# Optimization experiments

Measured on AMD Instinct MI355X. Metric: run time of the kernel, lower is better.

## Reference

```python
import jax, jax.numpy as jnp
import numpy as np

H = 32          # encoding_size
VC = 128        # char vocab (both languages)
TC = 24         # max chars per word
NW = 4096       # words per sentence side


def lstm_cell(x_t, h, c, Wih, Whh, b):
    g = x_t @ Wih.T + h @ Whh.T + b
    i, f, gg, o = jnp.split(g, 4, axis=-1)
    c2 = jax.nn.sigmoid(f) * c + jax.nn.sigmoid(i) * jnp.tanh(gg)
    h2 = jax.nn.sigmoid(o) * jnp.tanh(c2)
    return h2, c2


def char_lstm_final(x, lens, Wih, Whh, b):
    """x: [N, T, V] packed char embeddings, lens: [N]. Returns final h [N, H].
    Mask-gated scan reproduces 'final hidden state at each word's true length'."""
    N, T, _ = x.shape
    Hh = Whh.shape[1]
    xt = jnp.swapaxes(x, 0, 1)                 # [T, N, V]
    ts = jnp.arange(T)

    def step(carry, inp):
        h, c = carry
        x_t, t = inp
        h2, c2 = lstm_cell(x_t, h, c, Wih, Whh, b)
        m = (t < lens)[:, None]
        return (jnp.where(m, h2, h), jnp.where(m, c2, c)), None

    z = jnp.zeros((N, Hh), x.dtype)
    (h, _), _ = jax.lax.scan(step, (z, z), (xt, ts))
    return h


def lstm_seq(xs, Wih, Whh, b):
    """xs: [T, D] (batch 1). Returns all hidden states [T, H]."""
    Hh = Whh.shape[1]

    def step(carry, x_t):
        h, c = carry
        h2, c2 = lstm_cell(x_t, h, c, Wih, Whh, b)
        return (h2, c2), h2

    z = jnp.zeros((Hh,), xs.dtype)
    _, ys = jax.lax.scan(step, (z, z), xs)
    return ys


def bilstm(xs, Wf_ih, Wf_hh, bf, Wb_ih, Wb_hh, bb):
    fwd = lstm_seq(xs, Wf_ih, Wf_hh, bf)
    bwd = lstm_seq(xs[::-1], Wb_ih, Wb_hh, bb)[::-1]
    return jnp.concatenate([fwd, bwd], axis=-1)   # [T, 2H]


def setup_inputs() -> dict:
    key = jax.random.key(0)
    ks = jax.random.split(key, 32)
    s = 0.1
    inp = {
        'e_chars': jax.random.randint(ks[0], (NW, TC), 0, VC, dtype=jnp.int32),
        'e_lens': jax.random.randint(ks[1], (NW,), 1, TC + 1, dtype=jnp.int32),
        'f_chars': jax.random.randint(ks[2], (NW, TC), 0, VC, dtype=jnp.int32),
        'f_lens': jax.random.randint(ks[3], (NW,), 1, TC + 1, dtype=jnp.int32),
        'diag': jax.random.uniform(ks[4], (NW, NW), dtype=jnp.float32),
        'embed_e': jax.random.normal(ks[5], (VC, VC), jnp.float32) * s,
        'embed_f': jax.random.normal(ks[6], (VC, VC), jnp.float32) * s,
        'e_char_Wih': jax.random.normal(ks[7], (4 * H, VC), jnp.float32) * s,
        'e_char_Whh': jax.random.normal(ks[8], (4 * H, H), jnp.float32) * s,
        'e_char_b': jax.random.normal(ks[9], (4 * H,), jnp.float32) * s,
        'f_char_Wih': jax.random.normal(ks[10], (4 * H, VC), jnp.float32) * s,
        'f_char_Whh': jax.random.normal(ks[11], (4 * H, H), jnp.float32) * s,
        'f_char_b': jax.random.normal(ks[12], (4 * H,), jnp.float32) * s,
        'e_fwd_Wih': jax.random.normal(ks[13], (4 * H, H), jnp.float32) * s,
        'e_fwd_Whh': jax.random.normal(ks[14], (4 * H, H), jnp.float32) * s,
        'e_fwd_b': jax.random.normal(ks[15], (4 * H,), jnp.float32) * s,
        'e_bwd_Wih': jax.random.normal(ks[16], (4 * H, H), jnp.float32) * s,
        'e_bwd_Whh': jax.random.normal(ks[17], (4 * H, H), jnp.float32) * s,
        'e_bwd_b': jax.random.normal(ks[18], (4 * H,), jnp.float32) * s,
        'f_fwd_Wih': jax.random.normal(ks[19], (4 * H, H), jnp.float32) * s,
        'f_fwd_Whh': jax.random.normal(ks[20], (4 * H, H), jnp.float32) * s,
        'f_fwd_b': jax.random.normal(ks[21], (4 * H,), jnp.float32) * s,
        'f_bwd_Wih': jax.random.normal(ks[22], (4 * H, H), jnp.float32) * s,
        'f_bwd_Whh': jax.random.normal(ks[23], (4 * H, H), jnp.float32) * s,
        'f_bwd_b': jax.random.normal(ks[24], (4 * H,), jnp.float32) * s,
    }
    return inp


def reference(e_chars, e_lens, f_chars, f_lens, diag,
              embed_e, embed_f,
              e_char_Wih, e_char_Whh, e_char_b,
              f_char_Wih, f_char_Whh, f_char_b,
              e_fwd_Wih, e_fwd_Whh, e_fwd_b,
              e_bwd_Wih, e_bwd_Whh, e_bwd_b,
              f_fwd_Wih, f_fwd_Whh, f_fwd_b,
              f_bwd_Wih, f_bwd_Whh, f_bwd_b):
    # per-word char-LSTM encodes (packed, mask-gated) -> [NW, H]
    e_seq = char_lstm_final(embed_e[e_chars], e_lens, e_char_Wih, e_char_Whh, e_char_b)
    f_seq = char_lstm_final(embed_f[f_chars], f_lens, f_char_Wih, f_char_Whh, f_char_b)
    # word-level bi-LSTM + sigmoid (module's self.tanh is nn.Sigmoid) -> [NW, 2H]
    e_enc = jax.nn.sigmoid(bilstm(e_seq, e_fwd_Wih, e_fwd_Whh, e_fwd_b,
                                  e_bwd_Wih, e_bwd_Whh, e_bwd_b))
    f_enc = jax.nn.sigmoid(bilstm(f_seq, f_fwd_Wih, f_fwd_Whh, f_fwd_b,
                                  f_bwd_Wih, f_bwd_Whh, f_bwd_b))
    # score_ij[i, j] = f_enc[i] . e_enc[j]  (single batched matmul; diag is unused, as in source)
    return f_enc @ e_enc.T
```

## Files before the change

### kernel.cpp

```cpp
#include <hip/hip_runtime.h>

#define kNW 4096
#define kTC 24
#define kCL 8
#define kBURN 32

typedef float v2f __attribute__((ext_vector_type(2)));
typedef int   v2i __attribute__((ext_vector_type(2)));

#define XE_OFF   0u
#define WH_OFF   32768u
#define ENC_OFF  2392064u

__device__ __forceinline__ float fsig(float x){
  return __builtin_amdgcn_rcpf(1.f + __builtin_amdgcn_exp2f(-1.44269504f * x));
}
__device__ __forceinline__ float ftanh_(float x){
  return fmaf(2.f, __builtin_amdgcn_rcpf(1.f + __builtin_amdgcn_exp2f(-2.88539008f * x)), -1.f);
}
__device__ __forceinline__ float rdlane(float v, int l){
  return __int_as_float(__builtin_amdgcn_readlane(__float_as_int(v), l));
}
__device__ __forceinline__ float xswap_lo2hi(float m){
#if defined(__has_builtin)
#if __has_builtin(__builtin_amdgcn_permlane32_swap)
  v2i r = __builtin_amdgcn_permlane32_swap(__float_as_int(m), __float_as_int(m), false, false);
  float a = __int_as_float(r.x), b = __int_as_float(r.y);
  return (a == m) ? b : a;
#else
  return __shfl(m, (int)(threadIdx.x & 31), 64);
#endif
#else
  return __shfl(m, (int)(threadIdx.x & 31), 64);
#endif
}

__global__ __launch_bounds__(256) void k_tables(
    const float* __restrict__ embed_e, const float* __restrict__ embed_f,
    const float* __restrict__ Wih_e, const float* __restrict__ b_e,
    const float* __restrict__ Wih_f, const float* __restrict__ b_f,
    float* __restrict__ ws)
{
  int lane = threadIdx.x & 63;
  int wv   = threadIdx.x >> 6;
  int gw   = blockIdx.x * 4 + wv;
  int side = gw >> 11;
  int c    = (gw & 2047) >> 4;
  int g0   = (gw & 15) * 8;
  const float* er = (side ? embed_f : embed_e) + c * 128;
  const float* Wih = side ? Wih_f : Wih_e;
  const float* bb  = side ? b_f   : b_e;
  float* X = ws + XE_OFF + side * 16384 + c * 128;

  float ea = er[lane], eb = er[lane + 64];
  #pragma unroll
  for (int i = 0; i < 8; ++i){
    const float* wr = Wih + (g0 + i) * 128;
    float p = ea * wr[lane] + eb * wr[lane + 64];
    #pragma unroll
    for (int m = 1; m < 64; m <<= 1) p += __shfl_xor(p, m, 64);
    if (lane == 0) X[g0 + i] = bb[g0 + i] + p;
  }
}

__global__ __launch_bounds__(64)
void k_char(
    const int* __restrict__ e_chars, const int* __restrict__ e_lens,
    const int* __restrict__ f_chars, const int* __restrict__ f_lens,
    const float* __restrict__ Whh_e, const float* __restrict__ Whh_f,
    float* __restrict__ ws)
{
  int side = blockIdx.y;
  const int* chars = side ? f_chars : e_chars;
  const int* lens  = side ? f_lens  : e_lens;
  const float* Whh = side ? Whh_f : Whh_e;
  const float* X   = ws + XE_OFF + side * 16384;
  float* wh        = ws + WH_OFF + side * 131072;

  int lane = threadIdx.x;
  int col  = lane & 31;
  int word = blockIdx.x;

  __shared__ __align__(16) float hl[32];

  v2f wA[16], wB[16];
  #pragma unroll
  for (int q = 0; q < 8; ++q){
    float4 a  = *(const float4*)(Whh + lane * 32 + q * 4);
    float4 b4 = *(const float4*)(Whh + (lane + 64) * 32 + q * 4);
    wA[q*2+0] = (v2f){a.x, a.y};   wA[q*2+1] = (v2f){a.z, a.w};
    wB[q*2+0] = (v2f){b4.x, b4.y}; wB[q*2+1] = (v2f){b4.z, b4.w};
  }
  if (lane < 32) hl[lane] = 0.f;

  float cst = 0.f, h2 = 0.f;
  int len = __builtin_amdgcn_readfirstlane(lens[word]);
  int cv = chars[word * kTC + (lane < kTC ? lane : kTC - 1)];
  auto CH = [&](int t){ int tc = t < len ? t : len - 1;
                        return __builtin_amdgcn_readlane(cv, tc); };

  float kB = (lane < 32) ? -2.88539008f : -1.44269504f;
  float cB = (lane < 32) ? 2.f : 1.f;
  float dB = (lane < 32) ? -1.f : 0.f;

  int c0 = CH(0);
  float xa = X[c0*128 + lane], xb = X[c0*128 + 64 + lane];

  for (int t = 0; t < len; ++t){
    float accA0 = xa, accB0 = xb;
    if (t + 1 < len){
      int cn = CH(t + 1);
      xa = X[cn*128 + lane]; xb = X[cn*128 + 64 + lane];
    }
    v2f qa0 = {0.f,0.f}, qa1 = {0.f,0.f}, qb0 = {0.f,0.f}, qb1 = {0.f,0.f};
    #pragma unroll
    for (int q = 0; q < 4; ++q){
      float4 hv = *(const float4*)(&hl[q * 4]);
      v2f h0 = (v2f){hv.x, hv.y}, h1 = (v2f){hv.z, hv.w};
      qa0 = __builtin_elementwise_fma(wA[q*2+0], h0, qa0);
      qa0 = __builtin_elementwise_fma(wA[q*2+1], h1, qa0);
      qb0 = __builtin_elementwise_fma(wB[q*2+0], h0, qb0);
      qb0 = __builtin_elementwise_fma(wB[q*2+1], h1, qb0);
    }
    #pragma unroll
    for (int q = 4; q < 8; ++q){
      float4 hv = *(const float4*)(&hl[q * 4]);
      v2f h0 = (v2f){hv.x, hv.y}, h1 = (v2f){hv.z, hv.w};
      qa1 = __builtin_elementwise_fma(wA[q*2+0], h0, qa1);
      qa1 = __builtin_elementwise_fma(wA[q*2+1], h1, qa1);
      qb1 = __builtin_elementwise_fma(wB[q*2+0], h0, qb1);
      qb1 = __builtin_elementwise_fma(wB[q*2+1], h1, qb1);
    }
    v2f va = qa0 + qa1, vb = qb0 + qb1;
    float accA = accA0 + va.x + va.y;
    float accB = accB0 + vb.x + vb.y;
    float sA = fsig(accA);
    float sB = fmaf(cB, __builtin_amdgcn_rcpf(1.f + __builtin_amdgcn_exp2f(kB * accB)), dB);
    float m   = sA * sB;
    float mex = xswap_lo2hi(m);
    cst = fmaf(sA, cst, mex);
    h2  = sB * ftanh_(cst);
    if (lane >= 32) hl[col] = h2;
  }
  if (lane >= 32) wh[(size_t)word * 32 + col] = h2;
}

__global__ __launch_bounds__(64) __attribute__((amdgpu_waves_per_eu(1, 2)))
void k_word_par(
    const float* __restrict__ Whh0, const float* __restrict__ Whh1,
    const float* __restrict__ Whh2, const float* __restrict__ Whh3,
    const float* __restrict__ Wih0, const float* __restrict__ b0,
    const float* __restrict__ Wih1, const float* __restrict__ b1,
    const float* __restrict__ Wih2, const float* __restrict__ b2,
    const float* __restrict__ Wih3, const float* __restrict__ b3,
    float* __restrict__ ws)
{
  int qk  = blockIdx.x;
  int dir = blockIdx.y;
  const float* Whh = dir==0?Whh0 : dir==1?Whh1 : dir==2?Whh2 : Whh3;
  const float* Wih = dir==0?Wih0 : dir==1?Wih1 : dir==2?Wih2 : Wih3;
  const float* bb  = dir==0?b0  : dir==1?b1  : dir==2?b2  : b3;
  int side = dir >> 1, bwd = dir & 1;
  const float* wh = ws + WH_OFF + side * 131072;
  float* enc = ws + ENC_OFF + side * 262144 + (bwd ? 32 : 0);
  int lane = threadIdx.x;

  __shared__ __align__(16) float whs[kBURN + kCL][32];

  int tauOut = qk * kCL;
  int tau0   = tauOut - kBURN; if (tau0 < 0) tau0 = 0;
  int tauEnd = tauOut + kCL;
  int n = tauEnd - tau0;

  auto POS = [&](int tau){ return bwd ? (kNW - 1 - tau) : tau; };

  for (int i = lane; i < n * 32; i += 64){
    int j = i >> 5, k = i & 31;
    whs[j][k] = wh[(size_t)POS(tau0 + j) * 32 + k];
  }

  v2f wA[16], wB[16], pA[16], pB[16];
  #pragma unroll
  for (int q = 0; q < 8; ++q){
    float4 a  = *(const float4*)(Whh + lane * 32 + q * 4);
    float4 b4 = *(const float4*)(Whh + (lane + 64) * 32 + q * 4);
    wA[q*2+0] = (v2f){a.x, a.y};   wA[q*2+1] = (v2f){a.z, a.w};
    wB[q*2+0] = (v2f){b4.x, b4.y}; wB[q*2+1] = (v2f){b4.z, b4.w};
    float4 c4 = *(const float4*)(Wih + lane * 32 + q * 4);
    float4 d4 = *(const float4*)(Wih + (lane + 64) * 32 + q * 4);
    pA[q*2+0] = (v2f){c4.x, c4.y}; pA[q*2+1] = (v2f){c4.z, c4.w};
    pB[q*2+0] = (v2f){d4.x, d4.y}; pB[q*2+1] = (v2f){d4.z, d4.w};
  }
  float bA = bb[lane], bB = bb[lane + 64];

  auto PDOT = [&](int j, float& rA, float& rB){
    v2f w2[16];
    #pragma unroll
    for (int q = 0; q < 8; ++q){
      float4 wv = *(const float4*)(&whs[j][q*4]);
      w2[q*2+0] = (v2f){wv.x, wv.y}; w2[q*2+1] = (v2f){wv.z, wv.w};
    }
    v2f s0 = {0.f,0.f}, s1 = {0.f,0.f}, t0 = {0.f,0.f}, t1 = {0.f,0.f};
    #pragma unroll
    for (int k = 0; k < 8; ++k){
      s0 = __builtin_elementwise_fma(pA[k],   w2[k],   s0);
      s1 = __builtin_elementwise_fma(pA[k+8], w2[k+8], s1);
      t0 = __builtin_elementwise_fma(pB[k],   w2[k],   t0);
      t1 = __builtin_elementwise_fma(pB[k+8], w2[k+8], t1);
    }
    v2f sv = s0 + s1, tv = t0 + t1;
    rA = sv.x + sv.y; rB = tv.x + tv.y;
  };

  v2f s2[16];
  #pragma unroll
  for (int k = 0; k < 16; ++k) s2[k] = (v2f){0.f, 0.f};
  float cst = 0.f;
  float kB = (lane < 32) ? -2.88539008f : -1.44269504f;
  float cB = (lane < 32) ? 2.f : 1.f;
  float dB = (lane < 32) ? -1.f : 0.f;

  float prA, prB;
  PDOT(0, prA, prB);
  for (int j = 0; j < n; ++j){
    int tau = tau0 + j;
    float nA = 0.f, nB = 0.f;
    if (j + 1 < n) PDOT(j + 1, nA, nB);
    v2f qa0 = {0.f,0.f}, qa1 = {0.f,0.f}, qb0 = {0.f,0.f}, qb1 = {0.f,0.f};
    #pragma unroll
    for (int k = 0; k < 8; ++k){
      qa0 = __builtin_elementwise_fma(wA[k],   s2[k],   qa0);
      qa1 = __builtin_elementwise_fma(wA[k+8], s2[k+8], qa1);
      qb0 = __builtin_elementwise_fma(wB[k],   s2[k],   qb0);
      qb1 = __builtin_elementwise_fma(wB[k+8], s2[k+8], qb1);
    }
    v2f va = (qa0 + qa1), vb = (qb0 + qb1);
    float accA = bA + prA + va.x + va.y;
    float accB = bB + prB + vb.x + vb.y;
    float sA = fsig(accA);
    float sB = fmaf(cB, __builtin_amdgcn_rcpf(1.f + __builtin_amdgcn_exp2f(kB * accB)), dB);
    float m   = sA * sB;
    float mex = xswap_lo2hi(m);
    cst = fmaf(sA, cst, mex);
    float h2 = sB * ftanh_(cst);
    if (lane >= 32 && tau >= tauOut)
      enc[(size_t)POS(tau) * 64 + (lane - 32)] = fsig(h2);
    #pragma unroll
    for (int k = 0; k < 16; ++k){
      s2[k].x = rdlane(h2, 32 + 2*k);
      s2[k].y = rdlane(h2, 32 + 2*k + 1);
    }
    prA = nA; prB = nB;
  }
}

__global__ __launch_bounds__(256) __attribute__((amdgpu_waves_per_eu(2, 4)))
void k_mm(const float* __restrict__ ws, float* __restrict__ out)
{
  const float* e_enc = ws + ENC_OFF;
  const float* f_enc = ws + ENC_OFF + 262144;
  __shared__ __align__(16) float fS[64][128];
  __shared__ __align__(16) float eS[64][128];
  int t = threadIdx.x;
  int row0 = blockIdx.y * 128;
  int col0 = blockIdx.x * 128;
  {
    int r = t & 127, kh = t >> 7;
    const float* fsrc = f_enc + (size_t)(row0 + r) * 64 + kh * 32;
    const float* esrc = e_enc + (size_t)(col0 + r) * 64 + kh * 32;
    #pragma unroll
    for (int q = 0; q < 8; ++q){
      float4 v = *(const float4*)(fsrc + q * 4);
      int k = kh * 32 + q * 4;
      fS[k+0][r] = v.x; fS[k+1][r] = v.y; fS[k+2][r] = v.z; fS[k+3][r] = v.w;
      float4 u = *(const float4*)(esrc + q * 4);
      eS[k+0][r] = u.x; eS[k+1][r] = u.y; eS[k+2][r] = u.z; eS[k+3][r] = u.w;
    }
  }
  __syncthreads();
  int tx = t & 15, ty = t >> 4;
  int r0 = ty * 8, c0 = tx * 8;
  v2f acc2[8][4];
  #pragma unroll
  for (int i = 0; i < 8; ++i)
    #pragma unroll
    for (int j = 0; j < 4; ++j) acc2[i][j] = (v2f){0.f, 0.f};

  #pragma unroll 4
  for (int k = 0; k < 64; ++k){
    float4 fa = *(const float4*)(&fS[k][r0]);
    float4 fb = *(const float4*)(&fS[k][r0 + 4]);
    float4 ea = *(const float4*)(&eS[k][c0]);
    float4 eb = *(const float4*)(&eS[k][c0 + 4]);
    float fr[8] = {fa.x, fa.y, fa.z, fa.w, fb.x, fb.y, fb.z, fb.w};
    v2f e2[4] = {(v2f){ea.x, ea.y}, (v2f){ea.z, ea.w},
                 (v2f){eb.x, eb.y}, (v2f){eb.z, eb.w}};
    #pragma unroll
    for (int i = 0; i < 8; ++i){
      v2f f2 = (v2f){fr[i], fr[i]};
      #pragma unroll
      for (int j = 0; j < 4; ++j)
        acc2[i][j] = __builtin_elementwise_fma(f2, e2[j], acc2[i][j]);
    }
  }
  #pragma unroll
  for (int i = 0; i < 8; ++i){
    float* dst = out + (size_t)(row0 + r0 + i) * 4096 + col0 + c0;
    *(float4*)(dst)     = make_float4(acc2[i][0].x, acc2[i][0].y, acc2[i][1].x, acc2[i][1].y);
    *(float4*)(dst + 4) = make_float4(acc2[i][2].x, acc2[i][2].y, acc2[i][3].x, acc2[i][3].y);
  }
}

extern "C" void kernel_launch(void* const* d_in, const int* in_sizes, int n_in,
                              void* d_out, int out_size, void* d_ws, size_t ws_size,
                              hipStream_t stream)
{
  const int* e_chars = (const int*)d_in[0];
  const int* e_lens  = (const int*)d_in[1];
  const int* f_chars = (const int*)d_in[2];
  const int* f_lens  = (const int*)d_in[3];
  const float* embed_e = (const float*)d_in[5];
  const float* embed_f = (const float*)d_in[6];
  const float* eC_ih = (const float*)d_in[7];
  const float* eC_hh = (const float*)d_in[8];
  const float* eC_b  = (const float*)d_in[9];
  const float* fC_ih = (const float*)d_in[10];
  const float* fC_hh = (const float*)d_in[11];
  const float* fC_b  = (const float*)d_in[12];
  const float* efw_ih = (const float*)d_in[13];
  const float* efw_hh = (const float*)d_in[14];
  const float* efw_b  = (const float*)d_in[15];
  const float* ebw_ih = (const float*)d_in[16];
  const float* ebw_hh = (const float*)d_in[17];
  const float* ebw_b  = (const float*)d_in[18];
  const float* ffw_ih = (const float*)d_in[19];
  const float* ffw_hh = (const float*)d_in[20];
  const float* ffw_b  = (const float*)d_in[21];
  const float* fbw_ih = (const float*)d_in[22];
  const float* fbw_hh = (const float*)d_in[23];
  const float* fbw_b  = (const float*)d_in[24];
  float* ws  = (float*)d_ws;
  float* out = (float*)d_out;

  hipLaunchKernelGGL(k_tables, dim3(1024), dim3(256), 0, stream,
                     embed_e, embed_f, eC_ih, eC_b, fC_ih, fC_b, ws);
  hipLaunchKernelGGL(k_char, dim3(4096, 2), dim3(64), 0, stream,
                     e_chars, e_lens, f_chars, f_lens, eC_hh, fC_hh, ws);
  hipLaunchKernelGGL(k_word_par, dim3(kNW / kCL, 4), dim3(64), 0, stream,
                     efw_hh, ebw_hh, ffw_hh, fbw_hh,
                     efw_ih, efw_b, ebw_ih, ebw_b, ffw_ih, ffw_b, fbw_ih, fbw_b, ws);
  hipLaunchKernelGGL(k_mm, dim3(32, 32), dim3(256), 0, stream, ws, out);
}
```

Baseline: 108.7 us.

## Pack multiple words and chunks per block with LDS-staged LSTM weights

k_char now runs 256-thread blocks where each of 4 waves encodes 2 words in sequence. k_word_par packs 4 chunk-waves per block. Both kernels load the recurrent and input weight matrices once per block into padded shared memory and read them from there, instead of each 64-thread block fetching them from global memory. This is meant to cut block-launch count and repeated global weight reads. The trade-off is a longer serial per-wave chain in k_char, fewer independent waves to hide latency, and extra block barriers.

```diff
diff --git a/kernel.cpp b/kernel.cpp
--- a/kernel.cpp
+++ b/kernel.cpp
@@ -63,7 +63,7 @@
   }
 }
 
-__global__ __launch_bounds__(64)
+__global__ __launch_bounds__(256)
 void k_char(
     const int* __restrict__ e_chars, const int* __restrict__ e_lens,
     const int* __restrict__ f_chars, const int* __restrict__ f_lens,
@@ -77,75 +77,85 @@
   const float* X   = ws + XE_OFF + side * 16384;
   float* wh        = ws + WH_OFF + side * 131072;
 
-  int lane = threadIdx.x;
+  int tid  = threadIdx.x;
+  int lane = tid & 63;
+  int wv   = tid >> 6;
   int col  = lane & 31;
-  int word = blockIdx.x;
-
-  __shared__ __align__(16) float hl[32];
+
+  __shared__ __align__(16) float wsh[128][36];
+  __shared__ __align__(16) float hl[4][32];
+
+  for (int i = tid; i < 4096; i += 256){
+    int r = i >> 5, c = i & 31;
+    wsh[r][c] = Whh[i];
+  }
+  __syncthreads();
 
   v2f wA[16], wB[16];
   #pragma unroll
   for (int q = 0; q < 8; ++q){
-    float4 a  = *(const float4*)(Whh + lane * 32 + q * 4);
-    float4 b4 = *(const float4*)(Whh + (lane + 64) * 32 + q * 4);
+    float4 a  = *(const float4*)(&wsh[lane][q * 4]);
+    float4 b4 = *(const float4*)(&wsh[lane + 64][q * 4]);
     wA[q*2+0] = (v2f){a.x, a.y};   wA[q*2+1] = (v2f){a.z, a.w};
     wB[q*2+0] = (v2f){b4.x, b4.y}; wB[q*2+1] = (v2f){b4.z, b4.w};
   }
-  if (lane < 32) hl[lane] = 0.f;
-
-  float cst = 0.f, h2 = 0.f;
-  int len = __builtin_amdgcn_readfirstlane(lens[word]);
-  int cv = chars[word * kTC + (lane < kTC ? lane : kTC - 1)];
-  auto CH = [&](int t){ int tc = t < len ? t : len - 1;
-                        return __builtin_amdgcn_readlane(cv, tc); };
 
   float kB = (lane < 32) ? -2.88539008f : -1.44269504f;
   float cB = (lane < 32) ? 2.f : 1.f;
   float dB = (lane < 32) ? -1.f : 0.f;
 
-  int c0 = CH(0);
-  float xa = X[c0*128 + lane], xb = X[c0*128 + 64 + lane];
-
-  for (int t = 0; t < len; ++t){
-    float accA0 = xa, accB0 = xb;
-    if (t + 1 < len){
-      int cn = CH(t + 1);
-      xa = X[cn*128 + lane]; xb = X[cn*128 + 64 + lane];
-    }
-    v2f qa0 = {0.f,0.f}, qa1 = {0.f,0.f}, qb0 = {0.f,0.f}, qb1 = {0.f,0.f};
-    #pragma unroll
-    for (int q = 0; q < 4; ++q){
-      float4 hv = *(const float4*)(&hl[q * 4]);
-      v2f h0 = (v2f){hv.x, hv.y}, h1 = (v2f){hv.z, hv.w};
-      qa0 = __builtin_elementwise_fma(wA[q*2+0], h0, qa0);
-      qa0 = __builtin_elementwise_fma(wA[q*2+1], h1, qa0);
-      qb0 = __builtin_elementwise_fma(wB[q*2+0], h0, qb0);
-      qb0 = __builtin_elementwise_fma(wB[q*2+1], h1, qb0);
-    }
-    #pragma unroll
-    for (int q = 4; q < 8; ++q){
-      float4 hv = *(const float4*)(&hl[q * 4]);
-      v2f h0 = (v2f){hv.x, hv.y}, h1 = (v2f){hv.z, hv.w};
-      qa1 = __builtin_elementwise_fma(wA[q*2+0], h0, qa1);
-      qa1 = __builtin_elementwise_fma(wA[q*2+1], h1, qa1);
-      qb1 = __builtin_elementwise_fma(wB[q*2+0], h0, qb1);
-      qb1 = __builtin_elementwise_fma(wB[q*2+1], h1, qb1);
-    }
-    v2f va = qa0 + qa1, vb = qb0 + qb1;
-    float accA = accA0 + va.x + va.y;
-    float accB = accB0 + vb.x + vb.y;
-    float sA = fsig(accA);
-    float sB = fmaf(cB, __builtin_amdgcn_rcpf(1.f + __builtin_amdgcn_exp2f(kB * accB)), dB);
-    float m   = sA * sB;
-    float mex = xswap_lo2hi(m);
-    cst = fmaf(sA, cst, mex);
-    h2  = sB * ftanh_(cst);
-    if (lane >= 32) hl[col] = h2;
-  }
-  if (lane >= 32) wh[(size_t)word * 32 + col] = h2;
-}
-
-__global__ __launch_bounds__(64) __attribute__((amdgpu_waves_per_eu(1, 2)))
+  #pragma unroll
+  for (int j = 0; j < 2; ++j){
+    int word = (blockIdx.x * 4 + wv) * 2 + j;
+    if (lane < 32) hl[wv][lane] = 0.f;
+    float cst = 0.f, h2 = 0.f;
+    int len = __builtin_amdgcn_readfirstlane(lens[word]);
+    int cv = chars[word * kTC + (lane < kTC ? lane : kTC - 1)];
+
+    int c0 = __builtin_amdgcn_readlane(cv, 0);
+    float xa = X[c0*128 + lane], xb = X[c0*128 + 64 + lane];
+
+    for (int t = 0; t < len; ++t){
+      float accA0 = xa, accB0 = xb;
+      if (t + 1 < len){
+        int cn = __builtin_amdgcn_readlane(cv, t + 1);
+        xa = X[cn*128 + lane]; xb = X[cn*128 + 64 + lane];
+      }
+      v2f qa0 = {0.f,0.f}, qa1 = {0.f,0.f}, qb0 = {0.f,0.f}, qb1 = {0.f,0.f};
+      #pragma unroll
+      for (int q = 0; q < 4; ++q){
+        float4 hv = *(const float4*)(&hl[wv][q * 4]);
+        v2f h0 = (v2f){hv.x, hv.y}, h1 = (v2f){hv.z, hv.w};
+        qa0 = __builtin_elementwise_fma(wA[q*2+0], h0, qa0);
+        qa0 = __builtin_elementwise_fma(wA[q*2+1], h1, qa0);
+        qb0 = __builtin_elementwise_fma(wB[q*2+0], h0, qb0);
+        qb0 = __builtin_elementwise_fma(wB[q*2+1], h1, qb0);
+      }
+      #pragma unroll
+      for (int q = 4; q < 8; ++q){
+        float4 hv = *(const float4*)(&hl[wv][q * 4]);
+        v2f h0 = (v2f){hv.x, hv.y}, h1 = (v2f){hv.z, hv.w};
+        qa1 = __builtin_elementwise_fma(wA[q*2+0], h0, qa1);
+        qa1 = __builtin_elementwise_fma(wA[q*2+1], h1, qa1);
+        qb1 = __builtin_elementwise_fma(wB[q*2+0], h0, qb1);
+        qb1 = __builtin_elementwise_fma(wB[q*2+1], h1, qb1);
+      }
+      v2f va = qa0 + qa1, vb = qb0 + qb1;
+      float accA = accA0 + va.x + va.y;
+      float accB = accB0 + vb.x + vb.y;
+      float sA = fsig(accA);
+      float sB = fmaf(cB, __builtin_amdgcn_rcpf(1.f + __builtin_amdgcn_exp2f(kB * accB)), dB);
+      float m   = sA * sB;
+      float mex = xswap_lo2hi(m);
+      cst = fmaf(sA, cst, mex);
+      h2  = sB * ftanh_(cst);
+      if (lane >= 32) hl[wv][col] = h2;
+    }
+    if (lane >= 32) wh[(size_t)word * 32 + col] = h2;
+  }
+}
+
+__global__ __launch_bounds__(256) __attribute__((amdgpu_waves_per_eu(1, 2)))
 void k_word_par(
     const float* __restrict__ Whh0, const float* __restrict__ Whh1,
     const float* __restrict__ Whh2, const float* __restrict__ Whh3,
@@ -155,7 +165,6 @@
     const float* __restrict__ Wih3, const float* __restrict__ b3,
     float* __restrict__ ws)
 {
-  int qk  = blockIdx.x;
   int dir = blockIdx.y;
   const float* Whh = dir==0?Whh0 : dir==1?Whh1 : dir==2?Whh2 : Whh3;
   const float* Wih = dir==0?Wih0 : dir==1?Wih1 : dir==2?Wih2 : Wih3;
@@ -163,9 +172,21 @@
   int side = dir >> 1, bwd = dir & 1;
   const float* wh = ws + WH_OFF + side * 131072;
   float* enc = ws + ENC_OFF + side * 262144 + (bwd ? 32 : 0);
-  int lane = threadIdx.x;
-
-  __shared__ __align__(16) float whs[kBURN + kCL][32];
+
+  int tid  = threadIdx.x;
+  int lane = tid & 63;
+  int wv   = tid >> 6;
+  int qk   = blockIdx.x * 4 + wv;
+
+  __shared__ __align__(16) float sWhh[128][36];
+  __shared__ __align__(16) float sWih[128][36];
+  __shared__ __align__(16) float whs[4][kBURN + kCL][32];
+
+  for (int i = tid; i < 4096; i += 256){
+    int r = i >> 5, c = i & 31;
+    sWhh[r][c] = Whh[i];
+    sWih[r][c] = Wih[i];
+  }
 
   int tauOut = qk * kCL;
   int tau0   = tauOut - kBURN; if (tau0 < 0) tau0 = 0;
@@ -176,18 +197,19 @@
 
   for (int i = lane; i < n * 32; i += 64){
     int j = i >> 5, k = i & 31;
-    whs[j][k] = wh[(size_t)POS(tau0 + j) * 32 + k];
-  }
+    whs[wv][j][k] = wh[(size_t)POS(tau0 + j) * 32 + k];
+  }
+  __syncthreads();
 
   v2f wA[16], wB[16], pA[16], pB[16];
   #pragma unroll
   for (int q = 0; q < 8; ++q){
-    float4 a  = *(const float4*)(Whh + lane * 32 + q * 4);
-    float4 b4 = *(const float4*)(Whh + (lane + 64) * 32 + q * 4);
+    float4 a  = *(const float4*)(&sWhh[lane][q * 4]);
+    float4 b4 = *(const float4*)(&sWhh[lane + 64][q * 4]);
     wA[q*2+0] = (v2f){a.x, a.y};   wA[q*2+1] = (v2f){a.z, a.w};
     wB[q*2+0] = (v2f){b4.x, b4.y}; wB[q*2+1] = (v2f){b4.z, b4.w};
-    float4 c4 = *(const float4*)(Wih + lane * 32 + q * 4);
-    float4 d4 = *(const float4*)(Wih + (lane + 64) * 32 + q * 4);
+    float4 c4 = *(const float4*)(&sWih[lane][q * 4]);
+    float4 d4 = *(const float4*)(&sWih[lane + 64][q * 4]);
     pA[q*2+0] = (v2f){c4.x, c4.y}; pA[q*2+1] = (v2f){c4.z, c4.w};
     pB[q*2+0] = (v2f){d4.x, d4.y}; pB[q*2+1] = (v2f){d4.z, d4.w};
   }
@@ -197,8 +219,8 @@
     v2f w2[16];
     #pragma unroll
     for (int q = 0; q < 8; ++q){
-      float4 wv = *(const float4*)(&whs[j][q*4]);
-      w2[q*2+0] = (v2f){wv.x, wv.y}; w2[q*2+1] = (v2f){wv.z, wv.w};
+      float4 wv4 = *(const float4*)(&whs[wv][j][q*4]);
+      w2[q*2+0] = (v2f){wv4.x, wv4.y}; w2[q*2+1] = (v2f){wv4.z, wv4.w};
     }
     v2f s0 = {0.f,0.f}, s1 = {0.f,0.f}, t0 = {0.f,0.f}, t1 = {0.f,0.f};
     #pragma unroll
@@ -344,9 +366,9 @@
 
   hipLaunchKernelGGL(k_tables, dim3(1024), dim3(256), 0, stream,
                      embed_e, embed_f, eC_ih, eC_b, fC_ih, fC_b, ws);
-  hipLaunchKernelGGL(k_char, dim3(4096, 2), dim3(64), 0, stream,
+  hipLaunchKernelGGL(k_char, dim3(512, 2), dim3(256), 0, stream,
                      e_chars, e_lens, f_chars, f_lens, eC_hh, fC_hh, ws);
-  hipLaunchKernelGGL(k_word_par, dim3(kNW / kCL, 4), dim3(64), 0, stream,
+  hipLaunchKernelGGL(k_word_par, dim3(kNW / kCL / 4, 4), dim3(256), 0, stream,
                      efw_hh, ebw_hh, ffw_hh, fbw_hh,
                      efw_ih, efw_b, ebw_ih, ebw_b, ffw_ih, ffw_b, fbw_ih, fbw_b, ws);
   hipLaunchKernelGGL(k_mm, dim3(32, 32), dim3(256), 0, stream, ws, out);
```

Result: faster. 101.6 us (-6.5%).
